# Kernel optimization log

Measured on AMD Instinct MI355X. Metric: run time of the kernel, lower is better.

The kernel has to match this reference:

```python
import jax, jax.numpy as jnp
from jax import lax
import numpy as np

B, V = 2, 6
C_IN, HF, WF = 64, 32, 56
ND = 32
BEV_C, BEV_H, BEV_W = 128, 128, 128
D_MIN, D_MAX, EXT = 1.0, 50.0, 20.0
BN_S = 1.0 / np.sqrt(1.0 + 1e-5)  # BatchNorm at init (running mean=0, var=1): x / sqrt(1+eps)

def _conv(x, w, b, pad):
    y = lax.conv_general_dilated(x, w, (1, 1), [(pad, pad), (pad, pad)],
                                 dimension_numbers=('NCHW', 'OIHW', 'NCHW'))
    return y + b[None, :, None, None]

def _gelu(x):
    return jax.nn.gelu(x, approximate=False)  # torch nn.GELU default = exact erf

def setup_inputs() -> dict:
    key = jax.random.key(0)
    ks = jax.random.split(key, 8)
    feat_maps = jax.random.normal(ks[0], (B, V, C_IN, HF, WF), jnp.float32)
    # pinhole intrinsics at feature-map scale
    f = 30.0
    K1 = np.array([[f, 0.0, WF / 2.0], [0.0, f, HF / 2.0], [0.0, 0.0, 1.0]], np.float32)
    K = jnp.broadcast_to(jnp.asarray(K1), (B, V, 3, 3))
    # cam->ego extrinsics: cam optical frame (x right, y down, z fwd) -> ego, yaw per camera
    R0 = np.array([[0., 0., 1.], [-1., 0., 0.], [0., -1., 0.]], np.float32)
    Ts = np.zeros((B, V, 4, 4), np.float32)
    for v in range(V):
        yaw = 2.0 * np.pi * v / V
        Rz = np.array([[np.cos(yaw), -np.sin(yaw), 0.], [np.sin(yaw), np.cos(yaw), 0.], [0., 0., 1.]], np.float32)
        Ts[:, v, :3, :3] = Rz @ R0
        Ts[:, v, :3, 3] = np.array([0.0, 0.0, 1.5], np.float32)
        Ts[:, v, 3, 3] = 1.0
    T = jnp.asarray(Ts)
    trust = jax.random.uniform(ks[1], (B, V), jnp.float32)
    depths = jnp.linspace(D_MIN, D_MAX, ND).astype(jnp.float32)
    s = 0.05
    dh_w1 = jax.random.normal(ks[2], (C_IN, C_IN, 3, 3), jnp.float32) * s
    dh_b1 = jnp.zeros((C_IN,), jnp.float32)
    dh_w2 = jax.random.normal(ks[3], (ND, C_IN, 1, 1), jnp.float32) * s
    dh_b2 = jnp.zeros((ND,), jnp.float32)
    fp_w = jax.random.normal(ks[4], (BEV_C, C_IN, 1, 1), jnp.float32) * s
    fp_b = jnp.zeros((BEV_C,), jnp.float32)
    br_w1 = jax.random.normal(ks[5], (BEV_C, BEV_C, 3, 3), jnp.float32) * s
    br_b1 = jnp.zeros((BEV_C,), jnp.float32)
    br_w2 = jax.random.normal(ks[6], (BEV_C, BEV_C, 3, 3), jnp.float32) * s
    br_b2 = jnp.zeros((BEV_C,), jnp.float32)
    return dict(feat_maps=feat_maps, K=K, T=T, trust=trust, depths=depths,
                dh_w1=dh_w1, dh_b1=dh_b1, dh_w2=dh_w2, dh_b2=dh_b2,
                fp_w=fp_w, fp_b=fp_b, br_w1=br_w1, br_b1=br_b1, br_w2=br_w2, br_b2=br_b2)

def reference(feat_maps, K, T, trust, depths, dh_w1, dh_b1, dh_w2, dh_b2, fp_w, fp_b, br_w1, br_b1, br_w2, br_b2):
    Bq, Vq, C, Hf, Wf = feat_maps.shape
    fm = feat_maps.reshape(Bq * Vq, C, Hf, Wf)
    # depth head -> per-pixel categorical over depth bins
    h = _gelu(_conv(fm, dh_w1, dh_b1, 1) * BN_S)
    depth_probs = jax.nn.softmax(_conv(h, dh_w2, dh_b2, 0), axis=1)   # (BV, ND, Hf, Wf)
    fp = _gelu(_conv(fm, fp_w, fp_b, 0) * BN_S)                       # (BV, Cb, Hf, Wf)
    feat_vox = fp[:, :, None] * depth_probs[:, None]                  # (BV, Cb, ND, Hf, Wf)
    Cb = fp.shape[1]
    Dn = depths.shape[0]
    Np = Hf * Wf * Dn
    # torch order: permute(0,2,3,1) -> (Cb, Hf, Wf, ND) flattened as (h, w, d)
    fv = feat_vox.transpose(0, 1, 3, 4, 2).reshape(Bq, Vq, Cb, Np)
    # frustum points in camera frame, same (pixel, depth) ordering
    yy, xx = jnp.meshgrid(jnp.arange(Hf, dtype=jnp.float32), jnp.arange(Wf, dtype=jnp.float32), indexing='ij')
    pix = jnp.stack([xx.ravel(), yy.ravel(), jnp.ones(Hf * Wf, jnp.float32)], axis=0)  # (3, P)
    Kinv = jnp.linalg.inv(K)                                          # (B,V,3,3)
    rays = jnp.einsum('bvij,jp->bvip', Kinv, pix)                     # (B,V,3,P)
    pts = rays[..., None] * depths                                    # (B,V,3,P,D)
    R = T[..., :3, :3]
    t = T[..., :3, 3]
    pts_ego = jnp.einsum('bvij,bvjpd->bvipd', R, pts) + t[..., None, None]
    x_e = pts_ego[:, :, 0].reshape(Bq, Vq, Np)
    y_e = pts_ego[:, :, 1].reshape(Bq, Vq, Np)
    col = ((x_e + EXT) / (2.0 * EXT) * (BEV_W - 1)).astype(jnp.int32)  # trunc-toward-zero == torch .long()
    row = ((y_e + EXT) / (2.0 * EXT) * (BEV_H - 1)).astype(jnp.int32)
    valid = (col >= 0) & (col < BEV_W) & (row >= 0) & (row < BEV_H)
    idx = jnp.where(valid, row * BEV_W + col, 0)                      # (B,V,Np)
    tw = lax.stop_gradient(trust)                                     # torch uses trust[b,v].item()
    contrib = fv * (tw[:, :, None, None] * valid[:, :, None, :].astype(fv.dtype))
    HWb = BEV_H * BEV_W
    idx_all = (idx + jnp.arange(Bq)[:, None, None] * HWb).reshape(-1)
    contrib_flat = contrib.transpose(2, 0, 1, 3).reshape(Cb, -1)      # (Cb, B*V*Np)
    bev_flat = jnp.zeros((Cb, Bq * HWb), fv.dtype).at[:, idx_all].add(contrib_flat)
    bev = bev_flat.reshape(Cb, Bq, BEV_H, BEV_W).transpose(1, 0, 2, 3)  # (B, Cb, H, W)
    h2 = _gelu(_conv(bev, br_w1, br_b1, 1) * BN_S)
    out = _gelu(_conv(h2, br_w2, br_b2, 1) * BN_S)
    return out
```

## Files before the change

kernel.cpp:

```cpp
#include <hip/hip_runtime.h>
#include <hip/hip_bf16.h>
#include <math.h>

#define BQ 2
#define NV 6
#define CIN 64
#define HF 32
#define WF 56
#define ND 32
#define BEVC 128
#define BEVH 128
#define BEVW 128
#define NPIX (HF*WF)
#define BV (BQ*NV)
#define NCOL (BV*WF)
#define NITEM (NCOL*ND)
#define NCELL (BQ*BEVH*BEVW)
#define EXT 20.0f
#define BN_S 0.99999500003749937f

typedef short bf16x8 __attribute__((ext_vector_type(8)));
typedef float f32x4 __attribute__((ext_vector_type(4)));

__device__ __forceinline__ float gelu(float x) {
    return 0.5f * x * (1.0f + erff(x * 0.70710678118654752f));
}

__device__ __forceinline__ unsigned short f2bf(float x) {
    union { float f; unsigned u; } v; v.f = x;
    unsigned r = v.u + 0x7FFFu + ((v.u >> 16) & 1u);
    return (unsigned short)(r >> 16);
}

__device__ void atomicAddBf16(unsigned short* addr, float val) {
    unsigned* base = (unsigned*)((size_t)addr & ~(size_t)3);
    bool hi = ((size_t)addr & 2) != 0;
    unsigned old = *base, assumed;
    do {
        assumed = old;
        unsigned short cur = hi ? (unsigned short)(assumed >> 16)
                                : (unsigned short)(assumed & 0xFFFF);
        union { unsigned u; float f; } vv; vv.u = ((unsigned)cur) << 16;
        unsigned short nb = f2bf(vv.f + val);
        unsigned newv = hi ? ((assumed & 0x0000FFFFu) | ((unsigned)nb << 16))
                           : ((assumed & 0xFFFF0000u) | (unsigned)nb);
        old = atomicCAS(base, assumed, newv);
    } while (old != assumed);
}

#define WF1_N (9*4*8*64*8)
#define WFP_N (2*8*64*8)
#define WFC1_N (9*2*4*64*8)
__global__ void k_wprep_all(const float* __restrict__ br_w1, const float* __restrict__ br_w2,
                            const float* __restrict__ fp_w, const float* __restrict__ dh_w1,
                            unsigned short* __restrict__ wf1, unsigned short* __restrict__ wf2,
                            unsigned short* __restrict__ wfp, unsigned short* __restrict__ wfc1,
                            int* __restrict__ count) {
    int gi = blockIdx.x * 256 + threadIdx.x;
    if (gi < NCELL) count[gi] = 0;

    int i = gi;
    if (i < 2 * WF1_N) {
        const float* w = (i < WF1_N) ? br_w1 : br_w2;
        unsigned short* wf = (i < WF1_N) ? wf1 : wf2;
        int j = (i < WF1_N) ? i : i - WF1_N;
        int e     = j & 7;
        int lane  = (j >> 3) & 63;
        int ntile = (j >> 9) & 7;
        int kstep = (j >> 12) & 3;
        int kpos  = j >> 14;
        int co = ntile * 16 + (lane & 15);
        int ci = kstep * 32 + ((lane >> 4) << 3) + e;
        wf[j] = f2bf(w[((size_t)co * BEVC + ci) * 9 + kpos]);
        return;
    }
    i -= 2 * WF1_N;
    if (i < WFP_N) {
        int e     = i & 7;
        int lane  = (i >> 3) & 63;
        int ntile = (i >> 9) & 7;
        int kstep = (i >> 12) & 1;
        int co = ntile * 16 + (lane & 15);
        int ci = kstep * 32 + ((lane >> 4) << 3) + e;
        wfp[i] = f2bf(fp_w[(size_t)co * CIN + ci]);
        return;
    }
    i -= WFP_N;
    if (i < WFC1_N) {
        int e     = i & 7;
        int lane  = (i >> 3) & 63;
        int ntile = (i >> 9) & 3;
        int kstep = (i >> 11) & 1;
        int kpos  = i >> 12;
        int co = ntile * 16 + (lane & 15);
        int ci = kstep * 32 + ((lane >> 4) << 3) + e;
        wfc1[i] = f2bf(dh_w1[((size_t)co * CIN + ci) * 9 + kpos]);
    }
}

#define C1_HW 18
#define C1_HP (C1_HW*6)
__global__ void k_conv1d(const float* __restrict__ fm, const unsigned short* __restrict__ wfrag,
                         const float* __restrict__ bias, const float* __restrict__ w2,
                         const float* __restrict__ b2, float* __restrict__ dp) {
    __shared__ float hbuf[64 * 65];
    __shared__ float wl2[ND * 65];
    __shared__ float bl2[ND];
    char* als = (char*)hbuf;

    int x0 = blockIdx.x * 16;
    int y0 = blockIdx.y * 4;
    int bv = blockIdx.z;
    const float* fmb = fm + (size_t)bv * CIN * NPIX;

    for (int i = threadIdx.x; i < ND * CIN; i += 256) {
        int d = i >> 6, ci = i & 63;
        wl2[d * 65 + ci] = w2[i];
    }
    if (threadIdx.x < ND) bl2[threadIdx.x] = b2[threadIdx.x];

    for (int i = threadIdx.x; i < C1_HP * 8; i += 256) {
        int pix = i >> 3, oct = i & 7;
        int r = pix / C1_HW, c = pix % C1_HW;
        int gy = y0 + r - 1, gx = x0 + c - 1;
        int4 w4 = {0, 0, 0, 0};
        if ((unsigned)gy < (unsigned)HF && (unsigned)gx < (unsigned)WF) {
            const float* p = fmb + (size_t)(oct * 8) * NPIX + gy * WF + gx;
            unsigned short b8[8];
            #pragma unroll
            for (int j = 0; j < 8; j++) b8[j] = f2bf(p[(size_t)j * NPIX]);
            w4.x = b8[0] | ((int)b8[1] << 16);
            w4.y = b8[2] | ((int)b8[3] << 16);
            w4.z = b8[4] | ((int)b8[5] << 16);
            w4.w = b8[6] | ((int)b8[7] << 16);
        }
        *(int4*)(als + pix * 128 + ((oct * 16) ^ ((pix & 7) << 4))) = w4;
    }
    __syncthreads();

    int wave = threadIdx.x >> 6;
    int lane = threadIdx.x & 63;
    int xx   = lane & 15;
    int kgrp = lane >> 4;

    const bf16x8* wv = (const bf16x8*)wfrag;
    float bi = bias[wave * 16 + xx];
    f32x4 acc[4];
    #pragma unroll
    for (int m = 0; m < 4; m++) acc[m] = (f32x4){bi, bi, bi, bi};

    for (int kpos = 0; kpos < 9; kpos++) {
        int dy = kpos / 3, dx = kpos % 3;
        #pragma unroll
        for (int kstep = 0; kstep < 2; kstep++) {
            bf16x8 b = wv[((kpos * 2 + kstep) * 4 + wave) * 64 + lane];
            #pragma unroll
            for (int m = 0; m < 4; m++) {
                int pix = (m + dy) * C1_HW + xx + dx;
                bf16x8 a = *(const bf16x8*)(als + pix * 128 +
                                            ((kstep * 64 + kgrp * 16) ^ ((pix & 7) << 4)));
                acc[m] = __builtin_amdgcn_mfma_f32_16x16x32_bf16(a, b, acc[m], 0, 0, 0);
            }
        }
    }
    __syncthreads();

    #pragma unroll
    for (int m = 0; m < 4; m++) {
        #pragma unroll
        for (int r = 0; r < 4; r++) {
            int pixel = m * 16 + kgrp * 4 + r;
            hbuf[pixel * 65 + wave * 16 + xx] = gelu(acc[m][r] * BN_S);
        }
    }
    __syncthreads();

    {
        int pixel = threadIdx.x >> 2;
        int part  = threadIdx.x & 3;
        int m = pixel >> 4, xcol = pixel & 15;
        int gy = y0 + m, gx = x0 + xcol;

        float hv[CIN];
        #pragma unroll
        for (int c4 = 0; c4 < CIN / 4; c4++) {
            float4 v = *(const float4*)&hbuf[pixel * 65 + c4 * 4];
            hv[c4 * 4 + 0] = v.x; hv[c4 * 4 + 1] = v.y;
            hv[c4 * 4 + 2] = v.z; hv[c4 * 4 + 3] = v.w;
        }
        float o[8];
        float mx = -1e30f;
        #pragma unroll
        for (int dd = 0; dd < 8; dd++) {
            int d = part * 8 + dd;
            float a = bl2[d];
            #pragma unroll
            for (int ci = 0; ci < CIN; ci++) a += wl2[d * 65 + ci] * hv[ci];
            o[dd] = a;
            mx = fmaxf(mx, a);
        }
        mx = fmaxf(mx, __shfl_xor(mx, 1));
        mx = fmaxf(mx, __shfl_xor(mx, 2));
        float s = 0.f;
        #pragma unroll
        for (int dd = 0; dd < 8; dd++) { o[dd] = expf(o[dd] - mx); s += o[dd]; }
        s += __shfl_xor(s, 1);
        s += __shfl_xor(s, 2);
        float inv = 1.0f / s;
        if (gx < WF) {
            float* op = dp + ((size_t)bv * NPIX + gy * WF + gx) * ND + part * 8;
            float4 v0 = {o[0] * inv, o[1] * inv, o[2] * inv, o[3] * inv};
            float4 v1 = {o[4] * inv, o[5] * inv, o[6] * inv, o[7] * inv};
            ((float4*)op)[0] = v0;
            ((float4*)op)[1] = v1;
        }
    }
}

__global__ void k_fp(const float* __restrict__ fm, const unsigned short* __restrict__ wfrag,
                     const float* __restrict__ bias, float* __restrict__ fp) {
    __shared__ char als[64 * 128];
    int p0 = blockIdx.x * 64;
    int bv = p0 / NPIX, pl0 = p0 % NPIX;
    const float* fmb = fm + (size_t)bv * CIN * NPIX + pl0;

    #pragma unroll
    for (int it = 0; it < 2; it++) {
        int t = threadIdx.x + it * 256;
        int oct = t >> 6, pix = t & 63;
        unsigned short b8[8];
        #pragma unroll
        for (int j = 0; j < 8; j++)
            b8[j] = f2bf(fmb[(size_t)(oct * 8 + j) * NPIX + pix]);
        int4 w4;
        w4.x = b8[0] | ((int)b8[1] << 16);
        w4.y = b8[2] | ((int)b8[3] << 16);
        w4.z = b8[4] | ((int)b8[5] << 16);
        w4.w = b8[6] | ((int)b8[7] << 16);
        *(int4*)(als + pix * 128 + ((oct * 16) ^ ((pix & 7) << 4))) = w4;
    }
    __syncthreads();

    int wave = threadIdx.x >> 6;
    int lane = threadIdx.x & 63;
    int xx   = lane & 15;
    int kgrp = lane >> 4;

    int prow = wave * 16 + xx;
    bf16x8 a0 = *(const bf16x8*)(als + prow * 128 + ((       kgrp * 16) ^ ((prow & 7) << 4)));
    bf16x8 a1 = *(const bf16x8*)(als + prow * 128 + ((64  +  kgrp * 16) ^ ((prow & 7) << 4)));

    const bf16x8* wv = (const bf16x8*)wfrag;

    #pragma unroll
    for (int n = 0; n < 8; n++) {
        float bi = bias[n * 16 + xx];
        f32x4 acc = (f32x4){bi, bi, bi, bi};
        bf16x8 b0 = wv[(0 * 8 + n) * 64 + lane];
        bf16x8 b1 = wv[(1 * 8 + n) * 64 + lane];
        acc = __builtin_amdgcn_mfma_f32_16x16x32_bf16(a0, b0, acc, 0, 0, 0);
        acc = __builtin_amdgcn_mfma_f32_16x16x32_bf16(a1, b1, acc, 0, 0, 0);
        #pragma unroll
        for (int r = 0; r < 4; r++) {
            int pixel = wave * 16 + kgrp * 4 + r;
            fp[(size_t)(p0 + pixel) * BEVC + n * 16 + xx] = gelu(acc[r] * BN_S);
        }
    }
}

struct Geo {
    float i00,i01,i02,i10,i11,i12,i20,i21,i22;
    float R00,R01,R02,t0,R10,R11,R12,t1;
};
__device__ __forceinline__ Geo load_geo(const float* Km, const float* Tm, int bv) {
    Geo G;
    const float* Kp = Km + bv * 9;
    float a = Kp[0], bb = Kp[1], cc = Kp[2];
    float d = Kp[3], e  = Kp[4], f  = Kp[5];
    float g = Kp[6], hh = Kp[7], ii = Kp[8];
    float A  = e * ii - f * hh;
    float Bm = -(d * ii - f * g);
    float Cm = d * hh - e * g;
    float det = a * A + bb * Bm + cc * Cm;
    float invd = 1.0f / det;
    G.i00 = A * invd;  G.i01 = -(bb * ii - cc * hh) * invd; G.i02 = (bb * f - cc * e) * invd;
    G.i10 = Bm * invd; G.i11 = (a * ii - cc * g) * invd;    G.i12 = -(a * f - cc * d) * invd;
    G.i20 = Cm * invd; G.i21 = -(a * hh - bb * g) * invd;   G.i22 = (a * e - bb * d) * invd;
    const float* Tp = Tm + bv * 16;
    G.R00 = Tp[0]; G.R01 = Tp[1]; G.R02 = Tp[2]; G.t0 = Tp[3];
    G.R10 = Tp[4]; G.R11 = Tp[5]; G.R12 = Tp[6]; G.t1 = Tp[7];
    return G;
}
__device__ __forceinline__ int geo_cell(const Geo& G, int px, int py, float dep) {
    float fx = (float)px, fy = (float)py;
    float r0 = G.i00 * fx + G.i01 * fy + G.i02;
    float r1 = G.i10 * fx + G.i11 * fy + G.i12;
    float r2 = G.i20 * fx + G.i21 * fy + G.i22;
    float xe = G.R00 * (r0 * dep) + G.R01 * (r1 * dep) + G.R02 * (r2 * dep) + G.t0;
    float ye = G.R10 * (r0 * dep) + G.R11 * (r1 * dep) + G.R12 * (r2 * dep) + G.t1;
    int col = (int)((xe + EXT) / (2.0f * EXT) * (float)(BEVW - 1));
    int row = (int)((ye + EXT) / (2.0f * EXT) * (float)(BEVH - 1));
    return (col >= 0 && col < BEVW && row >= 0 && row < BEVH) ? row * BEVW + col : -1;
}

__global__ void k_prered(const float* __restrict__ fp, const float* __restrict__ dp,
                         const float* __restrict__ Km, const float* __restrict__ Tm,
                         const float* __restrict__ trust, const float* __restrict__ depths,
                         float* __restrict__ M, int* __restrict__ cellidx,
                         int* __restrict__ count) {
    __shared__ float fpl[HF * BEVC];
    __shared__ float dpl[HF * ND];
    __shared__ int   celll[ND * HF];
    __shared__ int   uni[ND];

    int col = blockIdx.x;
    int bv = col / WF, px = col % WF;
    int b  = bv / NV;
    float tw = trust[bv];

    for (int i = threadIdx.x; i < HF * (BEVC / 4); i += 256) {
        int py = i >> 5, c4 = i & 31;
        float4 v = ((const float4*)(fp + ((size_t)bv * NPIX + py * WF + px) * BEVC))[c4];
        v.x *= tw; v.y *= tw; v.z *= tw; v.w *= tw;
        ((float4*)fpl)[py * 32 + c4] = v;
    }
    for (int i = threadIdx.x; i < HF * (ND / 4); i += 256) {
        int py = i >> 3, d4 = i & 7;
        ((float4*)dpl)[py * 8 + d4] =
            ((const float4*)(dp + ((size_t)bv * NPIX + py * WF + px) * ND))[d4];
    }

    Geo G = load_geo(Km, Tm, bv);
    for (int q = threadIdx.x; q < ND * HF; q += 256) {
        int di = q >> 5, py = q & 31;
        celll[q] = geo_cell(G, px, py, depths[di]);
    }
    __syncthreads();

    if (threadIdx.x < ND) {
        int di = threadIdx.x;
        int c0 = celll[di * HF];
        bool u = true;
        for (int py = 1; py < HF; py++) u &= (celll[di * HF + py] == c0);
        uni[di] = u ? c0 : -2;
    }
    __syncthreads();

    int c = threadIdx.x & 127, dg = threadIdx.x >> 7;
    float acc[16];
    #pragma unroll
    for (int k = 0; k < 16; k++) acc[k] = 0.f;
    for (int py = 0; py < HF; py++) {
        float fv = fpl[py * BEVC + c];
        #pragma unroll
        for (int k = 0; k < 16; k++)
            acc[k] += fv * dpl[py * ND + dg * 16 + k];
    }
    #pragma unroll
    for (int k = 0; k < 16; k++)
        M[((size_t)col * ND + dg * 16 + k) * BEVC + c] = acc[k];

    if (threadIdx.x < ND) {
        int u = uni[threadIdx.x];
        int id = (u >= 0) ? (b * (BEVH * BEVW) + u) : u;
        cellidx[col * ND + threadIdx.x] = id;
        if (id >= 0) atomicAdd(&count[id], 1);
    }
}

__global__ void k_scan(const int* __restrict__ count, int* __restrict__ offs,
                       int* __restrict__ cursor) {
    __shared__ int part[1024];
    int t = threadIdx.x;
    int base = t * 32;
    int loc[32];
    int s = 0;
    #pragma unroll
    for (int i = 0; i < 32; i++) { loc[i] = s; s += count[base + i]; }
    part[t] = s;
    __syncthreads();
    for (int off = 1; off < 1024; off <<= 1) {
        int v = (t >= off) ? part[t - off] : 0;
        __syncthreads();
        part[t] += v;
        __syncthreads();
    }
    int pre = (t == 0) ? 0 : part[t - 1];
    #pragma unroll
    for (int i = 0; i < 32; i++) {
        offs[base + i] = pre + loc[i];
        cursor[base + i] = pre + loc[i];
    }
    if (t == 1023) offs[NCELL] = pre + s;
}

__global__ void k_fill(const int* __restrict__ cellidx, int* __restrict__ cursor,
                       int* __restrict__ itemlist) {
    int i = blockIdx.x * 256 + threadIdx.x;
    if (i >= NITEM) return;
    int c = cellidx[i];
    if (c >= 0) {
        int p = atomicAdd(&cursor[c], 1);
        itemlist[p] = i;
    }
}

__global__ void k_gather(const float* __restrict__ M, const int* __restrict__ offs,
                         const int* __restrict__ itemlist, unsigned short* __restrict__ bev) {
    int cell = blockIdx.x;
    int s = offs[cell], e = offs[cell + 1];
    int c = threadIdx.x;
    float acc = 0.f;
    for (int j = s; j < e; j++) {
        int it = itemlist[j];
        acc += M[(size_t)it * BEVC + c];
    }
    bev[(size_t)cell * BEVC + c] = f2bf(acc);
}

__global__ void k_fallback(const float* __restrict__ fp, const float* __restrict__ dp,
                           const float* __restrict__ Km, const float* __restrict__ Tm,
                           const float* __restrict__ trust, const float* __restrict__ depths,
                           const int* __restrict__ cellidx, unsigned short* __restrict__ bev) {
    int col = blockIdx.x;
    bool any = false;
    for (int di = 0; di < ND; di++) any |= (cellidx[col * ND + di] == -2);
    if (!any) return;

    int bv = col / WF, px = col % WF;
    int b  = bv / NV;
    float tw = trust[bv];
    Geo G = load_geo(Km, Tm, bv);
    int c = threadIdx.x;
    unsigned short* bevb = bev + (size_t)b * BEVH * BEVW * BEVC;
    for (int di = 0; di < ND; di++) {
        if (cellidx[col * ND + di] != -2) continue;
        float dep = depths[di];
        for (int py = 0; py < HF; py++) {
            int cell = geo_cell(G, px, py, dep);
            if (cell >= 0) {
                float v = fp[((size_t)bv * NPIX + py * WF + px) * BEVC + c] * tw *
                          dp[((size_t)bv * NPIX + py * WF + px) * ND + di];
                atomicAddBf16(&bevb[(size_t)cell * BEVC + c], v);
            }
        }
    }
}

#define TX2 16
#define TY2 4
#define HALO_W 18
#define HP (HALO_W*6)

__device__ __forceinline__ int swz(int pix, int off) {
    return pix * 256 + (off ^ ((pix & 7) << 4));
}

template<int TO_MODE>
__global__ __launch_bounds__(256, 2)
void k_bevconv(const unsigned short* __restrict__ in_,
               const unsigned short* __restrict__ wfrag,
               const float* __restrict__ bias, void* __restrict__ out_) {
    __shared__ char ldsb[HP * 256];
    int bid = blockIdx.x;
    int id = (bid & 7) * 64 + (bid >> 3);
    int x0 = (id & 7) * TX2;
    int y0 = ((id >> 3) & 31) * TY2;
    int b  = id >> 8;

    for (int t = threadIdx.x; t < HP * 16; t += 256) {
        int pix = t >> 4, oct = t & 15;
        int r = pix / HALO_W, c = pix % HALO_W;
        int gy = y0 + r - 1, gx = x0 + c - 1;
        int4 w4 = {0, 0, 0, 0};
        if ((unsigned)gy < (unsigned)BEVH && (unsigned)gx < (unsigned)BEVW)
            w4 = *(const int4*)(in_ + ((size_t)(b * BEVH + gy) * BEVW + gx) * BEVC + oct * 8);
        *(int4*)(ldsb + swz(pix, oct * 16)) = w4;
    }

    int wave = threadIdx.x >> 6;
    int lane = threadIdx.x & 63;
    int xx   = lane & 15;
    int kgrp = lane >> 4;

    const bf16x8* wv = (const bf16x8*)wfrag;
    int wbase = wave * 2;

    bf16x8 wq[4][2];
    #pragma unroll
    for (int p = 0; p < 4; p++) {
        wq[p][0] = wv[(p * 8 + wbase + 0) * 64 + lane];
        wq[p][1] = wv[(p * 8 + wbase + 1) * 64 + lane];
    }

    f32x4 acc[TY2][2];
    {
        float b0 = bias[wave * 32 + xx];
        float b1 = bias[wave * 32 + 16 + xx];
        #pragma unroll
        for (int m = 0; m < TY2; m++) {
            acc[m][0] = (f32x4){b0, b0, b0, b0};
            acc[m][1] = (f32x4){b1, b1, b1, b1};
        }
    }
    __syncthreads();

    #pragma unroll
    for (int i = 0; i < 36; i++) {
        const int kpos = i >> 2, kstep = i & 3;
        const int dy = kpos / 3, dx = kpos % 3;
        bf16x8 b0 = wq[i & 3][0];
        bf16x8 b1 = wq[i & 3][1];
        if (i + 4 < 36) {
            wq[i & 3][0] = wv[((i + 4) * 8 + wbase + 0) * 64 + lane];
            wq[i & 3][1] = wv[((i + 4) * 8 + wbase + 1) * 64 + lane];
        }
        #pragma unroll
        for (int m = 0; m < TY2; m++) {
            bf16x8 a = *(const bf16x8*)(ldsb + swz((m + dy) * HALO_W + xx + dx,
                                                   kstep * 64 + kgrp * 16));
            acc[m][0] = __builtin_amdgcn_mfma_f32_16x16x32_bf16(a, b0, acc[m][0], 0, 0, 0);
            acc[m][1] = __builtin_amdgcn_mfma_f32_16x16x32_bf16(a, b1, acc[m][1], 0, 0, 0);
        }
    }
    __syncthreads();

    if (TO_MODE == 1) {
        unsigned short* hl = (unsigned short*)ldsb;
        #pragma unroll
        for (int m = 0; m < TY2; m++)
            #pragma unroll
            for (int n = 0; n < 2; n++)
                #pragma unroll
                for (int r = 0; r < 4; r++) {
                    int pid = m * 16 + kgrp * 4 + r;
                    hl[pid * 136 + wave * 32 + n * 16 + xx] = f2bf(gelu(acc[m][n][r] * BN_S));
                }
        __syncthreads();
        for (int t = threadIdx.x; t < 1024; t += 256) {
            int pid = t >> 4, oct = t & 15;
            int gy = y0 + (pid >> 4), gx = x0 + (pid & 15);
            *(int4*)((unsigned short*)out_ + ((size_t)(b * BEVH + gy) * BEVW + gx) * BEVC + oct * 8) =
                *(int4*)(hl + pid * 136 + oct * 8);
        }
    } else {
        float* fl = (float*)ldsb;
        #pragma unroll
        for (int half = 0; half < 2; half++) {
            if (half == 1) __syncthreads();
            if ((wave >> 1) == half) {
                #pragma unroll
                for (int m = 0; m < TY2; m++)
                    #pragma unroll
                    for (int n = 0; n < 2; n++)
                        #pragma unroll
                        for (int r = 0; r < 4; r++) {
                            int pid = m * 16 + kgrp * 4 + r;
                            fl[pid * 66 + (wave & 1) * 32 + n * 16 + xx] =
                                gelu(acc[m][n][r] * BN_S);
                        }
            }
            __syncthreads();
            for (int t = threadIdx.x; t < 1024; t += 256) {
                int l4 = t & 3, gyl = (t >> 2) & 3, col = t >> 4;
                int co = half * 64 + col;
                int gy = y0 + gyl;
                float4 v;
                v.x = fl[(gyl * 16 + l4 * 4 + 0) * 66 + col];
                v.y = fl[(gyl * 16 + l4 * 4 + 1) * 66 + col];
                v.z = fl[(gyl * 16 + l4 * 4 + 2) * 66 + col];
                v.w = fl[(gyl * 16 + l4 * 4 + 3) * 66 + col];
                *(float4*)((float*)out_ + (((size_t)b * BEVC + co) * BEVH + gy) * BEVW +
                           x0 + l4 * 4) = v;
            }
        }
    }
}

extern "C" void kernel_launch(void* const* d_in, const int* in_sizes, int n_in,
                              void* d_out, int out_size, void* d_ws, size_t ws_size,
                              hipStream_t stream) {
    const float* feat_maps = (const float*)d_in[0];
    const float* Km        = (const float*)d_in[1];
    const float* Tm        = (const float*)d_in[2];
    const float* trust     = (const float*)d_in[3];
    const float* depths    = (const float*)d_in[4];
    const float* dh_w1     = (const float*)d_in[5];
    const float* dh_b1     = (const float*)d_in[6];
    const float* dh_w2     = (const float*)d_in[7];
    const float* dh_b2     = (const float*)d_in[8];
    const float* fp_w      = (const float*)d_in[9];
    const float* fp_b      = (const float*)d_in[10];
    const float* br_w1     = (const float*)d_in[11];
    const float* br_b1     = (const float*)d_in[12];
    const float* br_w2     = (const float*)d_in[13];
    const float* br_b2     = (const float*)d_in[14];
    float* out = (float*)d_out;

    float* ws  = (float*)d_ws;
    float* dpb = ws;
    float* fpb = dpb + (size_t)BV * NPIX * ND;
    float* Mb  = fpb + (size_t)BV * NPIX * BEVC;
    unsigned short* bevb = (unsigned short*)(Mb + (size_t)NITEM * BEVC);
    unsigned short* h2b  = bevb + (size_t)NCELL * BEVC;
    unsigned short* wf1  = h2b + (size_t)NCELL * BEVC;
    unsigned short* wf2  = wf1 + (size_t)WF1_N;
    unsigned short* wfp  = wf2 + (size_t)WF1_N;
    unsigned short* wfc1 = wfp + WFP_N;
    int* cellidx  = (int*)(wfc1 + WFC1_N);
    int* count    = cellidx + NITEM;
    int* offs     = count + NCELL;
    int* cursor   = offs + NCELL + 1;
    int* itemlist = cursor + NCELL;

    {
        int total = 2 * WF1_N + WFP_N + WFC1_N;
        k_wprep_all<<<dim3((total + 255) / 256), dim3(256), 0, stream>>>(
            br_w1, br_w2, fp_w, dh_w1, wf1, wf2, wfp, wfc1, count);
    }

    k_conv1d<<<dim3(4, HF / 4, BV), dim3(256), 0, stream>>>(
        feat_maps, wfc1, dh_b1, dh_w2, dh_b2, dpb);

    k_fp<<<dim3(BV * NPIX / 64), dim3(256), 0, stream>>>(feat_maps, wfp, fp_b, fpb);

    k_prered<<<dim3(NCOL), dim3(256), 0, stream>>>(fpb, dpb, Km, Tm, trust, depths,
                                                   Mb, cellidx, count);
    k_scan<<<dim3(1), dim3(1024), 0, stream>>>(count, offs, cursor);
    k_fill<<<dim3((NITEM + 255) / 256), dim3(256), 0, stream>>>(cellidx, cursor, itemlist);
    k_gather<<<dim3(NCELL), dim3(BEVC), 0, stream>>>(Mb, offs, itemlist, bevb);
    k_fallback<<<dim3(NCOL), dim3(BEVC), 0, stream>>>(fpb, dpb, Km, Tm, trust, depths,
                                                      cellidx, bevb);

    k_bevconv<1><<<dim3(512), dim3(256), 0, stream>>>(bevb, wf1, br_b1, h2b);
    k_bevconv<2><<<dim3(512), dim3(256), 0, stream>>>(h2b, wf2, br_b2, out);
}
```

Before: 120.4 us.

## Fuse feature projection into depth conv and replace scan/fill with fixed buckets

```diff
diff --git a/kernel.cpp b/kernel.cpp
--- a/kernel.cpp
+++ b/kernel.cpp
@@ -16,6 +16,7 @@
 #define NCOL (BV*WF)
 #define NITEM (NCOL*ND)
 #define NCELL (BQ*BEVH*BEVW)
+#define BCAP 16
 #define EXT 20.0f
 #define BN_S 0.99999500003749937f
 
@@ -55,9 +56,10 @@
                             const float* __restrict__ fp_w, const float* __restrict__ dh_w1,
                             unsigned short* __restrict__ wf1, unsigned short* __restrict__ wf2,
                             unsigned short* __restrict__ wfp, unsigned short* __restrict__ wfc1,
-                            int* __restrict__ count) {
+                            int* __restrict__ count, int* __restrict__ ovf_n) {
     int gi = blockIdx.x * 256 + threadIdx.x;
     if (gi < NCELL) count[gi] = 0;
+    if (gi == 0) *ovf_n = 0;
 
     int i = gi;
     if (i < 2 * WF1_N) {
@@ -100,9 +102,11 @@
 
 #define C1_HW 18
 #define C1_HP (C1_HW*6)
-__global__ void k_conv1d(const float* __restrict__ fm, const unsigned short* __restrict__ wfrag,
-                         const float* __restrict__ bias, const float* __restrict__ w2,
-                         const float* __restrict__ b2, float* __restrict__ dp) {
+__global__ void k_conv1dfp(const float* __restrict__ fm, const unsigned short* __restrict__ wfrag,
+                           const float* __restrict__ bias, const float* __restrict__ w2,
+                           const float* __restrict__ b2, const unsigned short* __restrict__ wfp,
+                           const float* __restrict__ fp_b,
+                           float* __restrict__ dp, float* __restrict__ fpb) {
     __shared__ float hbuf[64 * 65];
     __shared__ float wl2[ND * 65];
     __shared__ float bl2[ND];
@@ -163,6 +167,29 @@
             }
         }
     }
+
+    {
+        const bf16x8* wvp = (const bf16x8*)wfp;
+        int hpix = (wave + 1) * C1_HW + xx + 1;
+        bf16x8 fa0 = *(const bf16x8*)(als + hpix * 128 +
+                                      ((       kgrp * 16) ^ ((hpix & 7) << 4)));
+        bf16x8 fa1 = *(const bf16x8*)(als + hpix * 128 +
+                                      ((64 +   kgrp * 16) ^ ((hpix & 7) << 4)));
+        #pragma unroll
+        for (int n = 0; n < 8; n++) {
+            float fb = fp_b[n * 16 + xx];
+            f32x4 facc = (f32x4){fb, fb, fb, fb};
+            facc = __builtin_amdgcn_mfma_f32_16x16x32_bf16(fa0, wvp[(0 * 8 + n) * 64 + lane], facc, 0, 0, 0);
+            facc = __builtin_amdgcn_mfma_f32_16x16x32_bf16(fa1, wvp[(1 * 8 + n) * 64 + lane], facc, 0, 0, 0);
+            #pragma unroll
+            for (int r = 0; r < 4; r++) {
+                int gx = x0 + kgrp * 4 + r;
+                if (gx < WF)
+                    fpb[((size_t)bv * NPIX + (y0 + wave) * WF + gx) * BEVC + n * 16 + xx] =
+                        gelu(facc[r] * BN_S);
+            }
+        }
+    }
     __syncthreads();
 
     #pragma unroll
@@ -213,57 +240,6 @@
             float4 v1 = {o[4] * inv, o[5] * inv, o[6] * inv, o[7] * inv};
             ((float4*)op)[0] = v0;
             ((float4*)op)[1] = v1;
-        }
-    }
-}
-
-__global__ void k_fp(const float* __restrict__ fm, const unsigned short* __restrict__ wfrag,
-                     const float* __restrict__ bias, float* __restrict__ fp) {
-    __shared__ char als[64 * 128];
-    int p0 = blockIdx.x * 64;
-    int bv = p0 / NPIX, pl0 = p0 % NPIX;
-    const float* fmb = fm + (size_t)bv * CIN * NPIX + pl0;
-
-    #pragma unroll
-    for (int it = 0; it < 2; it++) {
-        int t = threadIdx.x + it * 256;
-        int oct = t >> 6, pix = t & 63;
-        unsigned short b8[8];
-        #pragma unroll
-        for (int j = 0; j < 8; j++)
-            b8[j] = f2bf(fmb[(size_t)(oct * 8 + j) * NPIX + pix]);
-        int4 w4;
-        w4.x = b8[0] | ((int)b8[1] << 16);
-        w4.y = b8[2] | ((int)b8[3] << 16);
-        w4.z = b8[4] | ((int)b8[5] << 16);
-        w4.w = b8[6] | ((int)b8[7] << 16);
-        *(int4*)(als + pix * 128 + ((oct * 16) ^ ((pix & 7) << 4))) = w4;
-    }
-    __syncthreads();
-
-    int wave = threadIdx.x >> 6;
-    int lane = threadIdx.x & 63;
-    int xx   = lane & 15;
-    int kgrp = lane >> 4;
-
-    int prow = wave * 16 + xx;
-    bf16x8 a0 = *(const bf16x8*)(als + prow * 128 + ((       kgrp * 16) ^ ((prow & 7) << 4)));
-    bf16x8 a1 = *(const bf16x8*)(als + prow * 128 + ((64  +  kgrp * 16) ^ ((prow & 7) << 4)));
-
-    const bf16x8* wv = (const bf16x8*)wfrag;
-
-    #pragma unroll
-    for (int n = 0; n < 8; n++) {
-        float bi = bias[n * 16 + xx];
-        f32x4 acc = (f32x4){bi, bi, bi, bi};
-        bf16x8 b0 = wv[(0 * 8 + n) * 64 + lane];
-        bf16x8 b1 = wv[(1 * 8 + n) * 64 + lane];
-        acc = __builtin_amdgcn_mfma_f32_16x16x32_bf16(a0, b0, acc, 0, 0, 0);
-        acc = __builtin_amdgcn_mfma_f32_16x16x32_bf16(a1, b1, acc, 0, 0, 0);
-        #pragma unroll
-        for (int r = 0; r < 4; r++) {
-            int pixel = wave * 16 + kgrp * 4 + r;
-            fp[(size_t)(p0 + pixel) * BEVC + n * 16 + xx] = gelu(acc[r] * BN_S);
         }
     }
 }
@@ -307,7 +283,8 @@
                          const float* __restrict__ Km, const float* __restrict__ Tm,
                          const float* __restrict__ trust, const float* __restrict__ depths,
                          float* __restrict__ M, int* __restrict__ cellidx,
-                         int* __restrict__ count) {
+                         int* __restrict__ count, int* __restrict__ bucket,
+                         int* __restrict__ ovf, int* __restrict__ ovf_n) {
     __shared__ float fpl[HF * BEVC];
     __shared__ float dpl[HF * ND];
     __shared__ int   celll[ND * HF];
@@ -363,59 +340,40 @@
     if (threadIdx.x < ND) {
         int u = uni[threadIdx.x];
         int id = (u >= 0) ? (b * (BEVH * BEVW) + u) : u;
-        cellidx[col * ND + threadIdx.x] = id;
-        if (id >= 0) atomicAdd(&count[id], 1);
-    }
-}
-
-__global__ void k_scan(const int* __restrict__ count, int* __restrict__ offs,
-                       int* __restrict__ cursor) {
-    __shared__ int part[1024];
-    int t = threadIdx.x;
-    int base = t * 32;
-    int loc[32];
-    int s = 0;
-    #pragma unroll
-    for (int i = 0; i < 32; i++) { loc[i] = s; s += count[base + i]; }
-    part[t] = s;
-    __syncthreads();
-    for (int off = 1; off < 1024; off <<= 1) {
-        int v = (t >= off) ? part[t - off] : 0;
-        __syncthreads();
-        part[t] += v;
-        __syncthreads();
-    }
-    int pre = (t == 0) ? 0 : part[t - 1];
-    #pragma unroll
-    for (int i = 0; i < 32; i++) {
-        offs[base + i] = pre + loc[i];
-        cursor[base + i] = pre + loc[i];
-    }
-    if (t == 1023) offs[NCELL] = pre + s;
-}
-
-__global__ void k_fill(const int* __restrict__ cellidx, int* __restrict__ cursor,
-                       int* __restrict__ itemlist) {
-    int i = blockIdx.x * 256 + threadIdx.x;
-    if (i >= NITEM) return;
-    int c = cellidx[i];
-    if (c >= 0) {
-        int p = atomicAdd(&cursor[c], 1);
-        itemlist[p] = i;
-    }
-}
-
-__global__ void k_gather(const float* __restrict__ M, const int* __restrict__ offs,
-                         const int* __restrict__ itemlist, unsigned short* __restrict__ bev) {
+        int item = col * ND + threadIdx.x;
+        cellidx[item] = id;
+        if (id >= 0) {
+            int slot = atomicAdd(&count[id], 1);
+            if (slot < BCAP) bucket[id * BCAP + slot] = item;
+            else             ovf[atomicAdd(ovf_n, 1)] = item;
+        }
+    }
+}
+
+__global__ void k_gather(const float* __restrict__ M, const int* __restrict__ count,
+                         const int* __restrict__ bucket, unsigned short* __restrict__ bev) {
     int cell = blockIdx.x;
-    int s = offs[cell], e = offs[cell + 1];
+    int n = count[cell];
+    if (n > BCAP) n = BCAP;
     int c = threadIdx.x;
     float acc = 0.f;
-    for (int j = s; j < e; j++) {
-        int it = itemlist[j];
+    for (int j = 0; j < n; j++) {
+        int it = bucket[cell * BCAP + j];
         acc += M[(size_t)it * BEVC + c];
     }
     bev[(size_t)cell * BEVC + c] = f2bf(acc);
+}
+
+__global__ void k_ovf(const float* __restrict__ M, const int* __restrict__ cellidx,
+                      const int* __restrict__ ovf, const int* __restrict__ ovf_n,
+                      unsigned short* __restrict__ bev) {
+    int no = *ovf_n;
+    int c = threadIdx.x;
+    for (int i = blockIdx.x; i < no; i += gridDim.x) {
+        int it = ovf[i];
+        int cell = cellidx[it];
+        atomicAddBf16(&bev[(size_t)cell * BEVC + c], M[(size_t)it * BEVC + c]);
+    }
 }
 
 __global__ void k_fallback(const float* __restrict__ fp, const float* __restrict__ dp,
@@ -609,26 +567,23 @@
     unsigned short* wfc1 = wfp + WFP_N;
     int* cellidx  = (int*)(wfc1 + WFC1_N);
     int* count    = cellidx + NITEM;
-    int* offs     = count + NCELL;
-    int* cursor   = offs + NCELL + 1;
-    int* itemlist = cursor + NCELL;
+    int* bucket   = count + NCELL;
+    int* ovf      = bucket + NCELL * BCAP;
+    int* ovf_n    = ovf + NITEM;
 
     {
         int total = 2 * WF1_N + WFP_N + WFC1_N;
         k_wprep_all<<<dim3((total + 255) / 256), dim3(256), 0, stream>>>(
-            br_w1, br_w2, fp_w, dh_w1, wf1, wf2, wfp, wfc1, count);
-    }
-
-    k_conv1d<<<dim3(4, HF / 4, BV), dim3(256), 0, stream>>>(
-        feat_maps, wfc1, dh_b1, dh_w2, dh_b2, dpb);
-
-    k_fp<<<dim3(BV * NPIX / 64), dim3(256), 0, stream>>>(feat_maps, wfp, fp_b, fpb);
+            br_w1, br_w2, fp_w, dh_w1, wf1, wf2, wfp, wfc1, count, ovf_n);
+    }
+
+    k_conv1dfp<<<dim3(4, HF / 4, BV), dim3(256), 0, stream>>>(
+        feat_maps, wfc1, dh_b1, dh_w2, dh_b2, wfp, fp_b, dpb, fpb);
 
     k_prered<<<dim3(NCOL), dim3(256), 0, stream>>>(fpb, dpb, Km, Tm, trust, depths,
-                                                   Mb, cellidx, count);
-    k_scan<<<dim3(1), dim3(1024), 0, stream>>>(count, offs, cursor);
-    k_fill<<<dim3((NITEM + 255) / 256), dim3(256), 0, stream>>>(cellidx, cursor, itemlist);
-    k_gather<<<dim3(NCELL), dim3(BEVC), 0, stream>>>(Mb, offs, itemlist, bevb);
+                                                   Mb, cellidx, count, bucket, ovf, ovf_n);
+    k_gather<<<dim3(NCELL), dim3(BEVC), 0, stream>>>(Mb, count, bucket, bevb);
+    k_ovf<<<dim3(64), dim3(BEVC), 0, stream>>>(Mb, cellidx, ovf, ovf_n, bevb);
     k_fallback<<<dim3(NCOL), dim3(BEVC), 0, stream>>>(fpb, dpb, Km, Tm, trust, depths,
                                                       cellidx, bevb);
 
```

Result: faster. 111.1 us (median of 2 runs) (-7.7%).
